# Performance work log

Measured on AMD Instinct MI355X. Metric: run time of the kernel, lower is better.

Reference implementation:

```python
import jax, jax.numpy as jnp
import numpy as np

NUM_HEADS = 32
NUM_KV_HEADS = 8
HEAD_DIM = 128
ROPE_THETA = 10000.0


def rotate_half(x):
    x1, x2 = jnp.split(x, 2, axis=-1)
    return jnp.concatenate((-x2, x1), axis=-1)


def setup_inputs() -> dict:
    key = jax.random.key(0)
    ks = jax.random.split(key, 5)
    B, S, H = 1, 2048, 4096
    KV = NUM_KV_HEADS * HEAD_DIM
    return {
        "hidden_states": jax.random.normal(ks[0], (B, S, H), dtype=jnp.float32),
        "position_ids": jnp.arange(S, dtype=jnp.int64 if jax.config.jax_enable_x64 else jnp.int32)[None, :].repeat(B, axis=0),
        "Wq": jax.random.normal(ks[1], (H, H), dtype=jnp.float32) * 0.02,
        "Wk": jax.random.normal(ks[2], (KV, H), dtype=jnp.float32) * 0.02,
        "Wv": jax.random.normal(ks[3], (KV, H), dtype=jnp.float32) * 0.02,
        "Wo": jax.random.normal(ks[4], (H, H), dtype=jnp.float32) * 0.02,
    }


def reference(hidden_states, position_ids, Wq, Wk, Wv, Wo):
    B, S, H = hidden_states.shape
    nh, nkv, hd = NUM_HEADS, NUM_KV_HEADS, HEAD_DIM
    n_rep = nh // nkv

    # QKV projections (torch Linear: y = x @ W^T)
    q = jnp.einsum('bsh,oh->bso', hidden_states, Wq).reshape(B, S, nh, hd).transpose(0, 2, 1, 3)
    k = jnp.einsum('bsh,oh->bso', hidden_states, Wk).reshape(B, S, nkv, hd).transpose(0, 2, 1, 3)
    v = jnp.einsum('bsh,oh->bso', hidden_states, Wv).reshape(B, S, nkv, hd).transpose(0, 2, 1, 3)

    # RoPE: cos/sin [B, 1, S, hd]
    inv_freq = 1.0 / (ROPE_THETA ** (jnp.arange(0, hd, 2, dtype=jnp.float32) / hd))
    freqs = position_ids.astype(jnp.float32)[..., None] * inv_freq  # [B, S, hd/2]
    emb = jnp.concatenate((freqs, freqs), axis=-1)                  # [B, S, hd]
    cos = jnp.cos(emb)[:, None, :, :]
    sin = jnp.sin(emb)[:, None, :, :]
    q = q * cos + rotate_half(q) * sin
    k = k * cos + rotate_half(k) * sin

    # GQA repeat_kv: [B, nkv, S, hd] -> [B, nh, S, hd]
    k = jnp.repeat(k, n_rep, axis=1)
    v = jnp.repeat(v, n_rep, axis=1)

    # eager attention with causal mask, softmax in fp32
    scores = jnp.einsum('bhqd,bhkd->bhqk', q, k) / jnp.sqrt(jnp.float32(hd))
    causal = jnp.tril(jnp.ones((S, S), dtype=bool))
    scores = jnp.where(causal[None, None], scores, jnp.finfo(scores.dtype).min)
    probs = jax.nn.softmax(scores.astype(jnp.float32), axis=-1).astype(q.dtype)
    attn = jnp.einsum('bhqk,bhkd->bhqd', probs, v)

    out = attn.transpose(0, 2, 1, 3).reshape(B, S, nh * hd)
    return jnp.einsum('bso,ho->bsh', out, Wo)
```

## Files before the change

kernel.cpp:

```cpp
#include <hip/hip_runtime.h>

typedef __bf16 bf16x8 __attribute__((ext_vector_type(8)));
typedef float f32x4 __attribute__((ext_vector_type(4)));
typedef unsigned int u32x4 __attribute__((ext_vector_type(4)));
typedef unsigned short u16x4 __attribute__((ext_vector_type(4)));

#define S_LEN 2048
#define HDIM  4096
#define KVDIM 1024
#define NHEAD 32
#define NKV   8
#define QKVN  6144

__device__ __forceinline__ unsigned short f2b(float x) {
    unsigned int u = __builtin_bit_cast(unsigned int, x);
    u = (u + 0x7FFFu + ((u >> 16) & 1u)) >> 16;
    return (unsigned short)u;
}
__device__ __forceinline__ float b2f(unsigned short b) {
    unsigned int u = ((unsigned int)b) << 16;
    return __builtin_bit_cast(float, u);
}

__device__ __forceinline__ void gl_lds16(const void* g, void* s) {
    __builtin_amdgcn_global_load_lds(
        (const __attribute__((address_space(1))) unsigned int*)g,
        (__attribute__((address_space(3))) unsigned int*)s, 16, 0, 0);
}

__global__ void cvt_all(const float* __restrict__ hid, const float* __restrict__ Wq,
                        const float* __restrict__ Wk, const float* __restrict__ Wv,
                        unsigned short* __restrict__ hb, unsigned short* __restrict__ Wqkvb) {
    const int NH = S_LEN * HDIM / 4;
    const int NQ = HDIM * HDIM / 4;
    const int NK = KVDIM * HDIM / 4;
    int i = blockIdx.x * 256 + threadIdx.x;
    const float* src;
    unsigned short* dst;
    int off;
    if (i < NH) { src = hid; dst = hb; off = i; }
    else if (i < NH + NQ) { src = Wq; dst = Wqkvb; off = i - NH; }
    else if (i < NH + NQ + NK) { src = Wk; dst = Wqkvb + (size_t)HDIM * HDIM; off = i - NH - NQ; }
    else { src = Wv; dst = Wqkvb + (size_t)(HDIM + KVDIM) * HDIM; off = i - NH - NQ - NK; }
    f32x4 v = ((const f32x4*)src)[off];
    u16x4 o;
    o.x = f2b(v.x); o.y = f2b(v.y); o.z = f2b(v.z); o.w = f2b(v.w);
    ((u16x4*)dst)[off] = o;
}

__global__ void post_kernel(const float* __restrict__ Wo, unsigned short* __restrict__ Wob,
                            unsigned short* __restrict__ Q, unsigned short* __restrict__ Kc,
                            const int* __restrict__ pos_ids) {
    const int NWB = HDIM * HDIM / 4 / 256;
    if (blockIdx.x < NWB) {
        int i = blockIdx.x * 256 + threadIdx.x;
        f32x4 v = ((const f32x4*)Wo)[i];
        u16x4 o;
        o.x = f2b(v.x); o.y = f2b(v.y); o.z = f2b(v.z); o.w = f2b(v.w);
        ((u16x4*)Wob)[i] = o;
        return;
    }
    int tid = (blockIdx.x - NWB) * 256 + threadIdx.x;
    int j = tid & 63;
    int head = (tid >> 6) % (NHEAD + NKV);
    int s = tid / (64 * (NHEAD + NKV));
    float pos = (float)pos_ids[s];
    float inv = exp2f(-(float)j * 0.20762050593046f);
    float ang = pos * inv;
    float sn, cs;
    __sincosf(ang, &sn, &cs);
    unsigned short* p;
    if (head < NHEAD)
        p = Q + (size_t)s * HDIM + head * 128;
    else
        p = Kc + (size_t)s * KVDIM + (head - NHEAD) * 128;
    float x1 = b2f(p[j]), x2 = b2f(p[j + 64]);
    p[j] = f2b(x1 * cs - x2 * sn);
    p[j + 64] = f2b(x2 * cs + x1 * sn);
}

template <int MODE>
__device__ __forceinline__ void gemm_body(const unsigned short* __restrict__ A,
                                          const unsigned short* __restrict__ B,
                                          void* __restrict__ Cv,
                                          int M, int N, int K, int m0, int n0, int cn0,
                                          unsigned short (*As)[64], unsigned short (*Bs)[64]) {
    const int tid = threadIdx.x;
    const int w = tid >> 6, lane = tid & 63, quad = lane >> 4, l15 = lane & 15;
    const int wy = w >> 1, wx = w & 1;
    const int srowb = w * 32 + (lane >> 3);
    const int gchunk = (lane & 7) ^ (lane >> 3);
    const int lcol = (lane & 7) * 8;

    f32x4 acc[4][4] = {};

    for (int k0 = 0; k0 < K; k0 += 64) {
#pragma unroll
        for (int p = 0; p < 4; ++p) {
            int r = srowb + p * 8;
            gl_lds16(&A[(size_t)(m0 + r) * K + k0 + gchunk * 8], &As[r][lcol]);
            gl_lds16(&B[(size_t)(n0 + r) * K + k0 + gchunk * 8], &Bs[r][lcol]);
        }
        __syncthreads();
#pragma unroll
        for (int t = 0; t < 2; ++t) {
            bf16x8 af[4], bfr[4];
#pragma unroll
            for (int mb = 0; mb < 4; ++mb)
                af[mb] = *(const bf16x8*)&As[wy * 64 + mb * 16 + l15][(((t * 4 + quad) ^ (l15 & 7)) * 8)];
#pragma unroll
            for (int nb = 0; nb < 4; ++nb)
                bfr[nb] = *(const bf16x8*)&Bs[wx * 64 + nb * 16 + l15][(((t * 4 + quad) ^ (l15 & 7)) * 8)];
#pragma unroll
            for (int mb = 0; mb < 4; ++mb)
#pragma unroll
                for (int nb = 0; nb < 4; ++nb)
                    acc[mb][nb] = __builtin_amdgcn_mfma_f32_16x16x32_bf16(af[mb], bfr[nb], acc[mb][nb], 0, 0, 0);
        }
        __syncthreads();
    }
#pragma unroll
    for (int mb = 0; mb < 4; ++mb)
#pragma unroll
        for (int nb = 0; nb < 4; ++nb)
#pragma unroll
            for (int r = 0; r < 4; ++r) {
                int row = m0 + wy * 64 + mb * 16 + quad * 4 + r;
                int col = cn0 + wx * 64 + nb * 16 + l15;
                float v = acc[mb][nb][r];
                if (MODE == 0)
                    ((unsigned short*)Cv)[(size_t)row * N + col] = f2b(v);
                else if (MODE == 1)
                    ((unsigned short*)Cv)[(size_t)col * M + row] = f2b(v);
                else
                    ((float*)Cv)[(size_t)row * N + col] = v;
            }
}

__global__ __launch_bounds__(256) void gemm_qkv(const unsigned short* __restrict__ A,
                                                const unsigned short* __restrict__ W,
                                                unsigned short* __restrict__ Q,
                                                unsigned short* __restrict__ Kc,
                                                unsigned short* __restrict__ Vt,
                                                int M, int K) {
    __shared__ unsigned short As[128][64];
    __shared__ unsigned short Bs[128][64];
    const int bx = blockIdx.x, m0 = blockIdx.y * 128, n0 = bx * 128;
    if (bx < 32)
        gemm_body<0>(A, W, Q, M, HDIM, K, m0, n0, n0, As, Bs);
    else if (bx < 40)
        gemm_body<0>(A, W, Kc, M, KVDIM, K, m0, n0, n0 - HDIM, As, Bs);
    else
        gemm_body<1>(A, W, Vt, M, KVDIM, K, m0, n0, n0 - HDIM - KVDIM, As, Bs);
}

template <int MODE>
__global__ __launch_bounds__(512) void gemm_wide(const unsigned short* __restrict__ A,
                                                 const unsigned short* __restrict__ B,
                                                 void* __restrict__ Cv, int M, int N, int K) {
    __shared__ unsigned short As[128][64];
    __shared__ unsigned short Bs[256][64];
    const int tid = threadIdx.x;
    const int w = tid >> 6, lane = tid & 63, quad = lane >> 4, l15 = lane & 15;
    const int wy = w >> 2, wx = w & 3;
    const int m0 = blockIdx.y * 128, n0 = blockIdx.x * 256;
    const int srow = w * 8 + (lane >> 3);
    const int gchunk = (lane & 7) ^ (lane >> 3);
    const int lcol = (lane & 7) * 8;

    f32x4 acc[4][4] = {};

    for (int k0 = 0; k0 < K; k0 += 64) {
#pragma unroll
        for (int p = 0; p < 2; ++p)
            gl_lds16(&A[(size_t)(m0 + p * 64 + srow) * K + k0 + gchunk * 8], &As[p * 64 + srow][lcol]);
#pragma unroll
        for (int p = 0; p < 4; ++p)
            gl_lds16(&B[(size_t)(n0 + p * 64 + srow) * K + k0 + gchunk * 8], &Bs[p * 64 + srow][lcol]);
        __syncthreads();
#pragma unroll
        for (int t = 0; t < 2; ++t) {
            bf16x8 af[4], bfr[4];
#pragma unroll
            for (int mb = 0; mb < 4; ++mb)
                af[mb] = *(const bf16x8*)&As[wy * 64 + mb * 16 + l15][(((t * 4 + quad) ^ (l15 & 7)) * 8)];
#pragma unroll
            for (int nb = 0; nb < 4; ++nb)
                bfr[nb] = *(const bf16x8*)&Bs[wx * 64 + nb * 16 + l15][(((t * 4 + quad) ^ (l15 & 7)) * 8)];
#pragma unroll
            for (int mb = 0; mb < 4; ++mb)
#pragma unroll
                for (int nb = 0; nb < 4; ++nb)
                    acc[mb][nb] = __builtin_amdgcn_mfma_f32_16x16x32_bf16(af[mb], bfr[nb], acc[mb][nb], 0, 0, 0);
        }
        __syncthreads();
    }
#pragma unroll
    for (int mb = 0; mb < 4; ++mb)
#pragma unroll
        for (int nb = 0; nb < 4; ++nb)
#pragma unroll
            for (int r = 0; r < 4; ++r) {
                int row = m0 + wy * 64 + mb * 16 + quad * 4 + r;
                int col = n0 + wx * 64 + nb * 16 + l15;
                float v = acc[mb][nb][r];
                if (MODE == 0)
                    ((unsigned short*)Cv)[(size_t)row * N + col] = f2b(v);
                else if (MODE == 2)
                    ((float*)Cv)[(size_t)row * N + col] = v;
            }
}

__global__ __launch_bounds__(256) void attn_fwd(const unsigned short* __restrict__ Q,
                                                const unsigned short* __restrict__ Kb,
                                                const unsigned short* __restrict__ Vt,
                                                unsigned short* __restrict__ O) {
    __shared__ unsigned short Ks[64][136];
    __shared__ unsigned short Vts[128][72];
    __shared__ unsigned short Ps[4][16][88];

    const int qblk = (gridDim.y - 1) - blockIdx.y;
    const int h = blockIdx.x, kvh = h >> 2;
    const int tid = threadIdx.x, w = tid >> 6, lane = tid & 63;
    const int quad = lane >> 4, l15 = lane & 15;
    const int qg = qblk * 64 + w * 16 + l15;

    bf16x8 aq[4];
#pragma unroll
    for (int t = 0; t < 4; ++t)
        aq[t] = *(const bf16x8*)&Q[(size_t)qg * HDIM + h * 128 + t * 32 + quad * 8];

    f32x4 o[8] = {};
    float m_s = -3.0e38f, l_s = 0.f;
    const float cexp = 0.08838834764831845f * 1.4426950408889634f;

    const int kr0 = tid >> 4, ksg = tid & 15;
    const int vr0 = tid >> 3, vsg = tid & 7;

    u32x4 kpre[4], vpre[4];
#pragma unroll
    for (int p = 0; p < 4; ++p) {
        kpre[p] = *(const u32x4*)&Kb[(size_t)(kr0 + p * 16) * KVDIM + kvh * 128 + ksg * 8];
        vpre[p] = *(const u32x4*)&Vt[(size_t)(kvh * 128 + vr0 + p * 32) * S_LEN + vsg * 8];
    }

    for (int kt = 0; kt <= qblk; ++kt) {
#pragma unroll
        for (int p = 0; p < 4; ++p) {
            *(u32x4*)&Ks[kr0 + p * 16][ksg * 8] = kpre[p];
            *(u32x4*)&Vts[vr0 + p * 32][vsg * 8] = vpre[p];
        }
        __syncthreads();
        if (kt < qblk) {
            const int k0n = kt * 64 + 64;
#pragma unroll
            for (int p = 0; p < 4; ++p) {
                kpre[p] = *(const u32x4*)&Kb[(size_t)(k0n + kr0 + p * 16) * KVDIM + kvh * 128 + ksg * 8];
                vpre[p] = *(const u32x4*)&Vt[(size_t)(kvh * 128 + vr0 + p * 32) * S_LEN + k0n + vsg * 8];
            }
        }

        f32x4 sc[4] = {};
        __builtin_amdgcn_s_setprio(1);
#pragma unroll
        for (int t = 0; t < 4; ++t)
#pragma unroll
            for (int mb = 0; mb < 4; ++mb) {
                bf16x8 ak = *(const bf16x8*)&Ks[mb * 16 + l15][t * 32 + quad * 8];
                sc[mb] = __builtin_amdgcn_mfma_f32_16x16x32_bf16(ak, aq[t], sc[mb], 0, 0, 0);
            }
        __builtin_amdgcn_s_setprio(0);

        float vv[16];
        if (kt == qblk) {
#pragma unroll
            for (int mb = 0; mb < 4; ++mb)
#pragma unroll
                for (int r = 0; r < 4; ++r) {
                    int kk = mb * 16 + quad * 4 + r;
                    vv[mb * 4 + r] = (kk <= w * 16 + l15) ? sc[mb][r] * cexp : -3.0e38f;
                }
        } else {
#pragma unroll
            for (int mb = 0; mb < 4; ++mb)
#pragma unroll
                for (int r = 0; r < 4; ++r)
                    vv[mb * 4 + r] = sc[mb][r] * cexp;
        }
        float m8[8];
#pragma unroll
        for (int i = 0; i < 8; ++i) m8[i] = fmaxf(vv[i], vv[i + 8]);
        float mx = fmaxf(fmaxf(fmaxf(m8[0], m8[1]), fmaxf(m8[2], m8[3])),
                         fmaxf(fmaxf(m8[4], m8[5]), fmaxf(m8[6], m8[7])));
        mx = fmaxf(mx, __shfl_xor(mx, 16, 64));
        mx = fmaxf(mx, __shfl_xor(mx, 32, 64));
        if (!__all(mx - m_s <= 8.0f)) {
            float mnew = fmaxf(m_s, mx);
            float alpha = exp2f(m_s - mnew);
            m_s = mnew;
            l_s *= alpha;
            float a4[4];
#pragma unroll
            for (int r = 0; r < 4; ++r) a4[r] = __shfl(alpha, quad * 20 + r, 64);
#pragma unroll
            for (int db = 0; db < 8; ++db)
#pragma unroll
                for (int r = 0; r < 4; ++r) o[db][r] *= a4[r];
        }
        float sum = 0.f;
        __bf16 pb[16] __attribute__((aligned(8)));
#pragma unroll
        for (int i = 0; i < 16; ++i) {
            float pp = exp2f(vv[i] - m_s);
            sum += pp;
            pb[i] = (__bf16)pp;
        }
        sum += __shfl_xor(sum, 16, 64);
        sum += __shfl_xor(sum, 32, 64);
        l_s += sum;
#pragma unroll
        for (int mb = 0; mb < 4; ++mb)
            *(u16x4*)&Ps[w][l15][mb * 16 + quad * 4] = *(const u16x4*)&pb[mb * 4];

        bf16x8 pa[2];
#pragma unroll
        for (int t = 0; t < 2; ++t)
            pa[t] = *(const bf16x8*)&Ps[w][l15][t * 32 + quad * 8];
        __builtin_amdgcn_s_setprio(1);
#pragma unroll
        for (int db = 0; db < 8; ++db)
#pragma unroll
            for (int t = 0; t < 2; ++t) {
                bf16x8 vb = *(const bf16x8*)&Vts[db * 16 + l15][t * 32 + quad * 8];
                o[db] = __builtin_amdgcn_mfma_f32_16x16x32_bf16(pa[t], vb, o[db], 0, 0, 0);
            }
        __builtin_amdgcn_s_setprio(0);
        __syncthreads();
    }

    float linv[4];
#pragma unroll
    for (int r = 0; r < 4; ++r) linv[r] = 1.0f / __shfl(l_s, quad * 20 + r, 64);
    const int qrow_base = qblk * 64 + w * 16 + quad * 4;
#pragma unroll
    for (int db = 0; db < 8; ++db)
#pragma unroll
        for (int r = 0; r < 4; ++r) {
            int row = qrow_base + r;
            int col = h * 128 + db * 16 + l15;
            O[(size_t)row * HDIM + col] = f2b(o[db][r] * linv[r]);
        }
}

extern "C" void kernel_launch(void* const* d_in, const int* in_sizes, int n_in,
                              void* d_out, int out_size, void* d_ws, size_t ws_size,
                              hipStream_t stream) {
    const float* hid = (const float*)d_in[0];
    const int* pos   = (const int*)d_in[1];
    const float* Wq  = (const float*)d_in[2];
    const float* Wk  = (const float*)d_in[3];
    const float* Wv  = (const float*)d_in[4];
    const float* Wo  = (const float*)d_in[5];
    float* out = (float*)d_out;

    char* ws = (char*)d_ws;
    unsigned short* hb    = (unsigned short*)(ws);
    unsigned short* Wqkvb = (unsigned short*)(ws + (16ull << 20));
    unsigned short* Wob   = (unsigned short*)(ws + (16ull << 20));
    unsigned short* Qw    = (unsigned short*)(ws + (64ull << 20));
    unsigned short* Kw    = (unsigned short*)(ws + (80ull << 20));
    unsigned short* Vtw   = (unsigned short*)(ws + (84ull << 20));
    unsigned short* attw  = hb;

    cvt_all<<<(S_LEN * HDIM / 4 + HDIM * HDIM / 4 + 2 * (KVDIM * HDIM / 4)) / 256, 256, 0, stream>>>(
        hid, Wq, Wk, Wv, hb, Wqkvb);

    gemm_qkv<<<dim3(QKVN / 128, S_LEN / 128), 256, 0, stream>>>(hb, Wqkvb, Qw, Kw, Vtw, S_LEN, HDIM);

    post_kernel<<<HDIM * HDIM / 4 / 256 + S_LEN * (NHEAD + NKV) * 64 / 256, 256, 0, stream>>>(
        Wo, Wob, Qw, Kw, pos);

    attn_fwd<<<dim3(NHEAD, S_LEN / 64), 256, 0, stream>>>(Qw, Kw, Vtw, attw);

    gemm_wide<2><<<dim3(HDIM / 256, S_LEN / 128), 512, 0, stream>>>(attw, Wob, out, S_LEN, HDIM, HDIM);
}
```

Before: 493.9 us.

## Fuse RoPE into QKV GEMM epilogue, fold Wo conversion, split-K output GEMM

RoPE is now applied in the QKV GEMM epilogue. The tile is staged through swizzled shared memory and each thread rotates half a row, so the separate post_kernel pass over Q and K is gone. The Wo bf16 conversion and the zeroing of the output are folded into the first conversion kernel when the workspace is large enough. The output projection becomes a 128x128 split-K (2-way) GEMM that accumulates with float atomicAdd. This aims to remove a kernel launch and extra memory passes and to improve occupancy of the final GEMM, at the cost of atomic traffic, nondeterministic summation order and extra epilogue work in the QKV GEMM.

Result: slower. 529.7 us (+7.3%).

```diff
diff --git a/kernel.cpp b/kernel.cpp
--- a/kernel.cpp
+++ b/kernel.cpp
@@ -28,9 +28,13 @@
         (__attribute__((address_space(3))) unsigned int*)s, 16, 0, 0);
 }
 
+__device__ __forceinline__ int csw(int r, int c) { return (c + 4 * r) & 127; }
+
 __global__ void cvt_all(const float* __restrict__ hid, const float* __restrict__ Wq,
                         const float* __restrict__ Wk, const float* __restrict__ Wv,
-                        unsigned short* __restrict__ hb, unsigned short* __restrict__ Wqkvb) {
+                        const float* __restrict__ Wo,
+                        unsigned short* __restrict__ hb, unsigned short* __restrict__ Wqkvb,
+                        unsigned short* __restrict__ Wob, float* __restrict__ outz, int nWo4) {
     const int NH = S_LEN * HDIM / 4;
     const int NQ = HDIM * HDIM / 4;
     const int NK = KVDIM * HDIM / 4;
@@ -41,42 +45,27 @@
     if (i < NH) { src = hid; dst = hb; off = i; }
     else if (i < NH + NQ) { src = Wq; dst = Wqkvb; off = i - NH; }
     else if (i < NH + NQ + NK) { src = Wk; dst = Wqkvb + (size_t)HDIM * HDIM; off = i - NH - NQ; }
-    else { src = Wv; dst = Wqkvb + (size_t)(HDIM + KVDIM) * HDIM; off = i - NH - NQ - NK; }
+    else if (i < NH + NQ + 2 * NK) { src = Wv; dst = Wqkvb + (size_t)(HDIM + KVDIM) * HDIM; off = i - NH - NQ - NK; }
+    else if (i < NH + NQ + 2 * NK + nWo4) { src = Wo; dst = Wob; off = i - NH - NQ - 2 * NK; }
+    else {
+        int z = i - (NH + NQ + 2 * NK + nWo4);
+        f32x4 zz = {0.f, 0.f, 0.f, 0.f};
+        ((f32x4*)outz)[z] = zz;
+        return;
+    }
     f32x4 v = ((const f32x4*)src)[off];
     u16x4 o;
     o.x = f2b(v.x); o.y = f2b(v.y); o.z = f2b(v.z); o.w = f2b(v.w);
     ((u16x4*)dst)[off] = o;
 }
 
-__global__ void post_kernel(const float* __restrict__ Wo, unsigned short* __restrict__ Wob,
-                            unsigned short* __restrict__ Q, unsigned short* __restrict__ Kc,
-                            const int* __restrict__ pos_ids) {
-    const int NWB = HDIM * HDIM / 4 / 256;
-    if (blockIdx.x < NWB) {
-        int i = blockIdx.x * 256 + threadIdx.x;
-        f32x4 v = ((const f32x4*)Wo)[i];
-        u16x4 o;
-        o.x = f2b(v.x); o.y = f2b(v.y); o.z = f2b(v.z); o.w = f2b(v.w);
-        ((u16x4*)Wob)[i] = o;
-        return;
-    }
-    int tid = (blockIdx.x - NWB) * 256 + threadIdx.x;
-    int j = tid & 63;
-    int head = (tid >> 6) % (NHEAD + NKV);
-    int s = tid / (64 * (NHEAD + NKV));
-    float pos = (float)pos_ids[s];
-    float inv = exp2f(-(float)j * 0.20762050593046f);
-    float ang = pos * inv;
-    float sn, cs;
-    __sincosf(ang, &sn, &cs);
-    unsigned short* p;
-    if (head < NHEAD)
-        p = Q + (size_t)s * HDIM + head * 128;
-    else
-        p = Kc + (size_t)s * KVDIM + (head - NHEAD) * 128;
-    float x1 = b2f(p[j]), x2 = b2f(p[j + 64]);
-    p[j] = f2b(x1 * cs - x2 * sn);
-    p[j + 64] = f2b(x2 * cs + x1 * sn);
+__global__ void cvt_kernel(const float* __restrict__ in, unsigned short* __restrict__ out, int n4) {
+    int i = blockIdx.x * 256 + threadIdx.x;
+    if (i >= n4) return;
+    f32x4 v = ((const f32x4*)in)[i];
+    u16x4 o;
+    o.x = f2b(v.x); o.y = f2b(v.y); o.z = f2b(v.z); o.w = f2b(v.w);
+    ((u16x4*)out)[i] = o;
 }
 
 template <int MODE>
@@ -84,7 +73,9 @@
                                           const unsigned short* __restrict__ B,
                                           void* __restrict__ Cv,
                                           int M, int N, int K, int m0, int n0, int cn0,
-                                          unsigned short (*As)[64], unsigned short (*Bs)[64]) {
+                                          unsigned short (*As)[64], unsigned short (*Bs)[64],
+                                          const int* __restrict__ pos_ids,
+                                          unsigned short* __restrict__ stash) {
     const int tid = threadIdx.x;
     const int w = tid >> 6, lane = tid & 63, quad = lane >> 4, l15 = lane & 15;
     const int wy = w >> 1, wx = w & 1;
@@ -119,6 +110,37 @@
         }
         __syncthreads();
     }
+
+    if (MODE == 3) {
+        unsigned short (*Cs)[128] = (unsigned short(*)[128])stash;
+#pragma unroll
+        for (int mb = 0; mb < 4; ++mb)
+#pragma unroll
+            for (int nb = 0; nb < 4; ++nb)
+#pragma unroll
+                for (int r = 0; r < 4; ++r) {
+                    int row = wy * 64 + mb * 16 + quad * 4 + r;
+                    int col = wx * 64 + nb * 16 + l15;
+                    Cs[row][csw(row, col)] = f2b(acc[mb][nb][r]);
+                }
+        __syncthreads();
+        const int rr = tid >> 1, jb = (tid & 1) << 5;
+        const float pos = (float)pos_ids[m0 + rr];
+        unsigned short* drow = (unsigned short*)Cv + (size_t)(m0 + rr) * N + cn0;
+#pragma unroll 8
+        for (int jj = 0; jj < 32; ++jj) {
+            int j = jb + jj;
+            float inv = exp2f(-(float)j * 0.20762050593046f);
+            float sn, cs;
+            __sincosf(pos * inv, &sn, &cs);
+            float x1 = b2f(Cs[rr][csw(rr, j)]);
+            float x2 = b2f(Cs[rr][csw(rr, j + 64)]);
+            drow[j] = f2b(x1 * cs - x2 * sn);
+            drow[j + 64] = f2b(x2 * cs + x1 * sn);
+        }
+        return;
+    }
+
 #pragma unroll
     for (int mb = 0; mb < 4; ++mb)
 #pragma unroll
@@ -132,8 +154,6 @@
                     ((unsigned short*)Cv)[(size_t)row * N + col] = f2b(v);
                 else if (MODE == 1)
                     ((unsigned short*)Cv)[(size_t)col * M + row] = f2b(v);
-                else
-                    ((float*)Cv)[(size_t)row * N + col] = v;
             }
 }
 
@@ -142,41 +162,44 @@
                                                 unsigned short* __restrict__ Q,
                                                 unsigned short* __restrict__ Kc,
                                                 unsigned short* __restrict__ Vt,
-                                                int M, int K) {
+                                                int M, int K, const int* __restrict__ pos) {
+    __shared__ unsigned short sm[2][128][64];
+    unsigned short (*As)[64] = sm[0];
+    unsigned short (*Bs)[64] = sm[1];
+    unsigned short* stash = &sm[0][0][0];
+    const int bx = blockIdx.x, m0 = blockIdx.y * 128, n0 = bx * 128;
+    if (bx < 32)
+        gemm_body<3>(A, W, Q, M, HDIM, K, m0, n0, n0, As, Bs, pos, stash);
+    else if (bx < 40)
+        gemm_body<3>(A, W, Kc, M, KVDIM, K, m0, n0, n0 - HDIM, As, Bs, pos, stash);
+    else
+        gemm_body<1>(A, W, Vt, M, KVDIM, K, m0, n0, n0 - HDIM - KVDIM, As, Bs, nullptr, nullptr);
+}
+
+__global__ __launch_bounds__(256) void gemm_out(const unsigned short* __restrict__ A,
+                                                const unsigned short* __restrict__ B,
+                                                float* __restrict__ C, int M, int N, int Kfull) {
     __shared__ unsigned short As[128][64];
     __shared__ unsigned short Bs[128][64];
-    const int bx = blockIdx.x, m0 = blockIdx.y * 128, n0 = bx * 128;
-    if (bx < 32)
-        gemm_body<0>(A, W, Q, M, HDIM, K, m0, n0, n0, As, Bs);
-    else if (bx < 40)
-        gemm_body<0>(A, W, Kc, M, KVDIM, K, m0, n0, n0 - HDIM, As, Bs);
-    else
-        gemm_body<1>(A, W, Vt, M, KVDIM, K, m0, n0, n0 - HDIM - KVDIM, As, Bs);
-}
-
-template <int MODE>
-__global__ __launch_bounds__(512) void gemm_wide(const unsigned short* __restrict__ A,
-                                                 const unsigned short* __restrict__ B,
-                                                 void* __restrict__ Cv, int M, int N, int K) {
-    __shared__ unsigned short As[128][64];
-    __shared__ unsigned short Bs[256][64];
     const int tid = threadIdx.x;
     const int w = tid >> 6, lane = tid & 63, quad = lane >> 4, l15 = lane & 15;
-    const int wy = w >> 2, wx = w & 3;
-    const int m0 = blockIdx.y * 128, n0 = blockIdx.x * 256;
-    const int srow = w * 8 + (lane >> 3);
+    const int wy = w >> 1, wx = w & 1;
+    const int srowb = w * 32 + (lane >> 3);
     const int gchunk = (lane & 7) ^ (lane >> 3);
     const int lcol = (lane & 7) * 8;
+    const int m0 = blockIdx.y * 128, n0 = blockIdx.x * 128;
+    const int khalf = Kfull >> 1;
+    const int kbeg = blockIdx.z * khalf, kend = kbeg + khalf;
 
     f32x4 acc[4][4] = {};
 
-    for (int k0 = 0; k0 < K; k0 += 64) {
-#pragma unroll
-        for (int p = 0; p < 2; ++p)
-            gl_lds16(&A[(size_t)(m0 + p * 64 + srow) * K + k0 + gchunk * 8], &As[p * 64 + srow][lcol]);
-#pragma unroll
-        for (int p = 0; p < 4; ++p)
-            gl_lds16(&B[(size_t)(n0 + p * 64 + srow) * K + k0 + gchunk * 8], &Bs[p * 64 + srow][lcol]);
+    for (int k0 = kbeg; k0 < kend; k0 += 64) {
+#pragma unroll
+        for (int p = 0; p < 4; ++p) {
+            int r = srowb + p * 8;
+            gl_lds16(&A[(size_t)(m0 + r) * Kfull + k0 + gchunk * 8], &As[r][lcol]);
+            gl_lds16(&B[(size_t)(n0 + r) * Kfull + k0 + gchunk * 8], &Bs[r][lcol]);
+        }
         __syncthreads();
 #pragma unroll
         for (int t = 0; t < 2; ++t) {
@@ -203,11 +226,7 @@
             for (int r = 0; r < 4; ++r) {
                 int row = m0 + wy * 64 + mb * 16 + quad * 4 + r;
                 int col = n0 + wx * 64 + nb * 16 + l15;
-                float v = acc[mb][nb][r];
-                if (MODE == 0)
-                    ((unsigned short*)Cv)[(size_t)row * N + col] = f2b(v);
-                else if (MODE == 2)
-                    ((float*)Cv)[(size_t)row * N + col] = v;
+                atomicAdd(&C[(size_t)row * N + col], acc[mb][nb][r]);
             }
 }
 
@@ -363,24 +382,30 @@
     const float* Wo  = (const float*)d_in[5];
     float* out = (float*)d_out;
 
+    const size_t MB = 1ull << 20;
     char* ws = (char*)d_ws;
     unsigned short* hb    = (unsigned short*)(ws);
-    unsigned short* Wqkvb = (unsigned short*)(ws + (16ull << 20));
-    unsigned short* Wob   = (unsigned short*)(ws + (16ull << 20));
-    unsigned short* Qw    = (unsigned short*)(ws + (64ull << 20));
-    unsigned short* Kw    = (unsigned short*)(ws + (80ull << 20));
-    unsigned short* Vtw   = (unsigned short*)(ws + (84ull << 20));
+    unsigned short* Wqkvb = (unsigned short*)(ws + 16 * MB);
+    unsigned short* Qw    = (unsigned short*)(ws + 64 * MB);
+    unsigned short* Kw    = (unsigned short*)(ws + 80 * MB);
+    unsigned short* Vtw   = (unsigned short*)(ws + 84 * MB);
     unsigned short* attw  = hb;
-
-    cvt_all<<<(S_LEN * HDIM / 4 + HDIM * HDIM / 4 + 2 * (KVDIM * HDIM / 4)) / 256, 256, 0, stream>>>(
-        hid, Wq, Wk, Wv, hb, Wqkvb);
-
-    gemm_qkv<<<dim3(QKVN / 128, S_LEN / 128), 256, 0, stream>>>(hb, Wqkvb, Qw, Kw, Vtw, S_LEN, HDIM);
-
-    post_kernel<<<HDIM * HDIM / 4 / 256 + S_LEN * (NHEAD + NKV) * 64 / 256, 256, 0, stream>>>(
-        Wo, Wob, Qw, Kw, pos);
+    const bool wofit = ws_size >= 120 * MB;
+    unsigned short* Wob = wofit ? (unsigned short*)(ws + 88 * MB) : Wqkvb;
+
+    const int nWo4 = wofit ? HDIM * HDIM / 4 : 0;
+    const int total4 = S_LEN * HDIM / 4 + HDIM * HDIM / 4 + 2 * (KVDIM * HDIM / 4)
+                     + nWo4 + S_LEN * HDIM / 4;
+    cvt_all<<<total4 / 256, 256, 0, stream>>>(hid, Wq, Wk, Wv, Wo, hb, Wqkvb, Wob, out, nWo4);
+
+    gemm_qkv<<<dim3(QKVN / 128, S_LEN / 128), 256, 0, stream>>>(hb, Wqkvb, Qw, Kw, Vtw,
+                                                                S_LEN, HDIM, pos);
+
+    if (!wofit)
+        cvt_kernel<<<HDIM * HDIM / 4 / 256, 256, 0, stream>>>(Wo, Wob, HDIM * HDIM / 4);
 
     attn_fwd<<<dim3(NHEAD, S_LEN / 64), 256, 0, stream>>>(Qw, Kw, Vtw, attw);
 
-    gemm_wide<2><<<dim3(HDIM / 256, S_LEN / 128), 512, 0, stream>>>(attw, Wob, out, S_LEN, HDIM, HDIM);
-}
+    gemm_out<<<dim3(HDIM / 128, S_LEN / 128, 2), 256, 0, stream>>>(attw, Wob, out,
+                                                                   S_LEN, HDIM, HDIM);
+}
```
